# Kernel optimization log

Measured on AMD Instinct MI355X. Metric: run time of the kernel, lower is better.

## Reference

```python
import jax, jax.numpy as jnp
import numpy as np

B = 8192          # batch of agents
K = 4             # max_neighbors
NUM_LANES = 12
LANE_F = 4        # obs_dim // num_lanes = 48 // 12
HEADS = 4
OUT = 32          # gat_output_dim per head
EMB = HEADS * OUT # 128, gat_per_lane_output / intersection emb dim
HID = 64          # graphsage_hidden_dim
GRU_H = 32        # gru_hidden_dim
ALPHA = 0.2       # leaky relu slope

# Lane cooperation: lanes of the same approach (4 approaches x 3 lanes) cooperate.
_blk = np.kron(np.eye(4), np.ones((3, 3))).astype(np.float32)
LANE_COOP = jnp.asarray(_blk)
LANE_CONF = jnp.asarray(1.0 - _blk)


def _gat_stream(x, W, a_src, a_dst, adj):
    # x: [N, 12, 4]; W: [H, 4, O]; a_*: [H, O]; adj: [12, 12]
    Wh = jnp.einsum('nlf,hfo->nhlo', x, W)                      # [N,H,12,O]
    e_s = jnp.einsum('nhlo,ho->nhl', Wh, a_src)
    e_d = jnp.einsum('nhlo,ho->nhl', Wh, a_dst)
    e = jax.nn.leaky_relu(e_s[..., :, None] + e_d[..., None, :], ALPHA)  # [N,H,12,12]
    e = jnp.where(adj[None, None] > 0, e, jnp.float32(-1e9))
    att = jax.nn.softmax(e, axis=-1)
    out = jnp.einsum('nhij,nhjo->niho', att, Wh)                # [N,12,H,O]
    return jax.nn.elu(out.reshape(out.shape[0], NUM_LANES, EMB))


def _gru_final(xs, Wih, Whh, bih, bhh):
    # xs: [K, B, HID] -> final hidden [B, GRU_H], torch GRU gate convention (r,z,n)
    def step(h, x):
        gi = x @ Wih + bih
        gh = h @ Whh + bhh
        i_r, i_z, i_n = jnp.split(gi, 3, axis=-1)
        h_r, h_z, h_n = jnp.split(gh, 3, axis=-1)
        r = jax.nn.sigmoid(i_r + h_r)
        z = jax.nn.sigmoid(i_z + h_z)
        n = jnp.tanh(i_n + r * h_n)
        return (1.0 - z) * n + z * h, None
    h0 = jnp.zeros((xs.shape[1], Whh.shape[0]), xs.dtype)
    hT, _ = jax.lax.scan(step, h0, xs)
    return hT


def setup_inputs() -> dict:
    key = jax.random.key(0)
    ks = jax.random.split(key, 24)
    rn = lambda k, s: (jax.random.normal(k, s, jnp.float32) * 0.1)
    z = lambda n: jnp.zeros((n,), jnp.float32)
    return {
        'self_features': jax.random.normal(ks[0], (B, 48), jnp.float32),
        'neighbor_features': jax.random.normal(ks[1], (B, K, 48), jnp.float32),
        'neighbor_mask': (jax.random.uniform(ks[2], (B, K)) > 0.25).astype(jnp.float32),
        'neighbor_directions': jax.random.randint(ks[3], (B, K), 0, 4).astype(jnp.float32) * 0.25,
        # dual-stream GAT params
        'W_coop': rn(ks[4], (HEADS, LANE_F, OUT)), 'a_src_coop': rn(ks[5], (HEADS, OUT)), 'a_dst_coop': rn(ks[6], (HEADS, OUT)),
        'W_conf': rn(ks[7], (HEADS, LANE_F, OUT)), 'a_src_conf': rn(ks[8], (HEADS, OUT)), 'a_dst_conf': rn(ks[9], (HEADS, OUT)),
        'W_fuse': rn(ks[10], (2 * EMB, EMB)), 'b_fuse': z(EMB),
        # GraphSAGE neighbor projection (+1 for direction feature)
        'W_proj': rn(ks[11], (EMB + 1, HID)), 'b_proj': z(HID),
        # BiGRU (fwd/bwd), torch layout transposed: Wih [HID,3H], Whh [H,3H]
        'Wih_f': rn(ks[12], (HID, 3 * GRU_H)), 'Whh_f': rn(ks[13], (GRU_H, 3 * GRU_H)), 'bih_f': z(3 * GRU_H), 'bhh_f': z(3 * GRU_H),
        'Wih_b': rn(ks[14], (HID, 3 * GRU_H)), 'Whh_b': rn(ks[15], (GRU_H, 3 * GRU_H)), 'bih_b': z(3 * GRU_H), 'bhh_b': z(3 * GRU_H),
        # combine self + BiGRU summary -> network embedding
        'W_out': rn(ks[16], (EMB + 2 * GRU_H, HID)), 'b_out': z(HID),
    }


def reference(self_features, neighbor_features, neighbor_mask, neighbor_directions,
              W_coop, a_src_coop, a_dst_coop, W_conf, a_src_conf, a_dst_conf,
              W_fuse, b_fuse, W_proj, b_proj,
              Wih_f, Whh_f, bih_f, bhh_f, Wih_b, Whh_b, bih_b, bhh_b,
              W_out, b_out):
    Bc, Kc = neighbor_features.shape[:2]
    # run dual-stream GAT on self + all neighbors in one batch of small lane graphs
    allx = jnp.concatenate([self_features[:, None, :], neighbor_features], axis=1)
    allx = allx.reshape(Bc * (Kc + 1), NUM_LANES, LANE_F)
    coop = _gat_stream(allx, W_coop, a_src_coop, a_dst_coop, LANE_COOP)
    conf = _gat_stream(allx, W_conf, a_src_conf, a_dst_conf, LANE_CONF)
    fused = jax.nn.elu(jnp.concatenate([coop, conf], axis=-1) @ W_fuse + b_fuse)  # [N,12,128]
    emb = fused.mean(axis=1).reshape(Bc, Kc + 1, EMB)  # mean pool over lanes
    self_emb = emb[:, 0]          # [B,128]
    nbr_emb = emb[:, 1:]          # [B,K,128]
    # GraphSAGE projection of neighbors (direction-aware), masked
    nbr_in = jnp.concatenate([nbr_emb, neighbor_directions[..., None]], axis=-1)
    x = jax.nn.relu(nbr_in @ W_proj + b_proj) * neighbor_mask[..., None]  # [B,K,HID]
    xs = jnp.swapaxes(x, 0, 1)    # [K,B,HID]
    h_f = _gru_final(xs, Wih_f, Whh_f, bih_f, bhh_f)
    h_b = _gru_final(xs[::-1], Wih_b, Whh_b, bih_b, bhh_b)
    net = jax.nn.relu(jnp.concatenate([self_emb, h_f, h_b], axis=-1) @ W_out + b_out)  # [B,64]
    return jnp.concatenate([self_emb, net], axis=-1)  # [B,192]
```

## Files before the change

### kernel.cpp

```cpp
#include <hip/hip_runtime.h>
#include <hip/hip_bf16.h>
#include <math.h>

typedef short short8 __attribute__((ext_vector_type(8)));
typedef float f32x4  __attribute__((ext_vector_type(4)));
typedef unsigned short u16x4 __attribute__((ext_vector_type(4)));

__device__ __forceinline__ unsigned short f2b(float f) {
  union { float f; unsigned int u; } x; x.f = f;
  return (unsigned short)((x.u + 0x7FFFu + ((x.u >> 16) & 1u)) >> 16);
}
__device__ __forceinline__ float b2f_u(unsigned short u) {
  union { unsigned int u; float f; } x; x.u = ((unsigned int)u) << 16;
  return x.f;
}
__device__ __forceinline__ unsigned int pkbf(float a, float b) {
  union { __hip_bfloat162 h; unsigned int u; } c;
  c.h = __float22bfloat162_rn(make_float2(a, b));
  return c.u;
}
__device__ __forceinline__ float sigm(float x) { return 1.f / (1.f + __expf(-x)); }
__device__ __forceinline__ float eluf(float v) {
  return v > 0.f ? v : (__expf(v) - 1.f);
}

__global__ __launch_bounds__(256) void prepack_kernel(
    const float* __restrict__ Wf,
    const float* __restrict__ Wc, const float* __restrict__ Wn,
    const float* __restrict__ as_c, const float* __restrict__ ad_c,
    const float* __restrict__ as_n, const float* __restrict__ ad_n,
    const float* __restrict__ Wproj,
    const float* __restrict__ Wih_f, const float* __restrict__ Wih_b,
    const float* __restrict__ Wout,
    const float* __restrict__ Whh_f, const float* __restrict__ Whh_b,
    unsigned short* __restrict__ fragB,
    unsigned short* __restrict__ fragWB,
    float* __restrict__ Wa,
    unsigned short* __restrict__ fragP,
    unsigned short* __restrict__ fragIH,
    unsigned short* __restrict__ fragO,
    unsigned short* __restrict__ fragHH)
{
  int e = blockIdx.x * 256 + threadIdx.x;
  unsigned short tmp[8];
  if (e < 4096) {
    int kb = e >> 9, tile = (e >> 6) & 7, lane = e & 63;
    int n = tile * 16 + (lane & 15);
    int kbase = kb * 32 + (lane >> 4) * 8;
#pragma unroll
    for (int j = 0; j < 8; j++) tmp[j] = f2b(Wf[(kbase + j) * 128 + n]);
    *(short8*)(fragB + e * 8) = *(short8*)tmp;
  } else if (e < 5120) {
    int i = e - 4096;
    int s = i >> 9, tile = (i >> 6) & 7, lane = i & 63;
    int c15 = lane & 15, quad = lane >> 4;
    int n = tile * 16 + c15;
    int h = n >> 5, o = n & 31;
    const float* W = s ? Wn : Wc;
#pragma unroll
    for (int j = 0; j < 8; j++) {
      int k = quad * 8 + j;
      tmp[j] = ((k >> 2) == h) ? f2b(W[h * 128 + (k & 3) * 32 + o])
                               : (unsigned short)0;
    }
    *(short8*)(fragWB + i * 8) = *(short8*)tmp;
  } else if (e < 5184) {
    int i = e - 5120;
    int s = i >> 5, d = (i >> 4) & 1, h = (i >> 2) & 3, f = i & 3;
    const float* W = s ? Wn : Wc;
    const float* a = s ? (d ? ad_n : as_n) : (d ? ad_c : as_c);
    float acc = 0.f;
#pragma unroll
    for (int o = 0; o < 32; o++) acc += W[h * 128 + f * 32 + o] * a[h * 32 + o];
    Wa[i] = acc;
  } else if (e < 6208) {
    int i = e - 5184;
    int kb = i >> 8, nt = (i >> 6) & 3, lane = i & 63;
    int c15 = lane & 15, quad = lane >> 4;
#pragma unroll
    for (int j = 0; j < 8; j++)
      tmp[j] = f2b(Wproj[(kb * 32 + quad * 8 + j) * 64 + nt * 16 + c15]);
    *(short8*)(fragP + i * 8) = *(short8*)tmp;
  } else if (e < 7744) {
    int i = e - 6208;
    int d = (i >= 768), r = i - d * 768;
    int kb = r / 384, nt = (r >> 6) % 6, lane = r & 63;
    int c15 = lane & 15, quad = lane >> 4;
    const float* W = d ? Wih_b : Wih_f;
#pragma unroll
    for (int j = 0; j < 8; j++)
      tmp[j] = f2b(W[(kb * 32 + quad * 8 + j) * 96 + nt * 16 + c15]);
    *(short8*)(fragIH + i * 8) = *(short8*)tmp;
  } else if (e < 9280) {
    int r = e - 7744;
    int kb = r >> 8, nt = (r >> 6) & 3, lane = r & 63;
    int c15 = lane & 15, quad = lane >> 4;
#pragma unroll
    for (int j = 0; j < 8; j++)
      tmp[j] = f2b(Wout[(kb * 32 + quad * 8 + j) * 64 + nt * 16 + c15]);
    *(short8*)(fragO + r * 8) = *(short8*)tmp;
  } else if (e < 10048) {
    int i = e - 9280;
    int d = i / 384, r = i - d * 384;
    int nt = r >> 6, lane = r & 63;
    int c15 = lane & 15, quad = lane >> 4;
    const float* W = d ? Whh_b : Whh_f;
#pragma unroll
    for (int j = 0; j < 8; j++)
      tmp[j] = f2b(W[(quad * 8 + j) * 96 + nt * 16 + c15]);
    *(short8*)(fragHH + i * 8) = *(short8*)tmp;
  }
}

__global__ __launch_bounds__(256) void gat_fuse_kernel(
    const float* __restrict__ self_f, const float* __restrict__ nbr_f,
    const float* __restrict__ Wa,
    const unsigned short* __restrict__ fragWB,
    const unsigned short* __restrict__ fragB,
    const float* __restrict__ b_fuse,
    float* __restrict__ emb)
{
  const int tid = threadIdx.x;
  const int w = tid >> 6, lane = tid & 63, c15 = lane & 15, quad = lane >> 4;
  const int n0 = blockIdx.x * 2;

  __shared__ __align__(16) float sxf[2][12][4];
  __shared__ float sWa[64];
  __shared__ float sed[2][2][4][12];
  __shared__ __align__(16) unsigned short sA[2][2][16][24];
  __shared__ __align__(16) unsigned short scatb[2][16][268];
  __shared__ float sbias[128];

  if (tid < 128) sbias[tid] = b_fuse[tid];
  if (tid < 64) sWa[tid] = Wa[tid];
  if (tid < 96) {
    int nd = tid / 48, f = tid - nd * 48;
    int nn = n0 + nd, b = nn / 5, slot = nn - b * 5;
    float v = (slot == 0) ? self_f[b * 48 + f]
                          : nbr_f[(b * 4 + slot - 1) * 48 + f];
    sxf[nd][f >> 2][f & 3] = v;
  }
  __syncthreads();

  const int g_q = w & 1, s_q = w >> 1;
  if (lane < 48) {
    int h = lane / 12, i = lane - h * 12;
    float es = 0.f, ed = 0.f;
#pragma unroll
    for (int f = 0; f < 4; f++) {
      float xv = sxf[g_q][i][f];
      es += xv * sWa[s_q * 32 + h * 4 + f];
      ed += xv * sWa[s_q * 32 + 16 + h * 4 + f];
    }
    sed[g_q][s_q][h][i] = ed;
    int blk = i / 3;
    float xa0 = 0.f, xa1 = 0.f, xa2 = 0.f, xa3 = 0.f;
    if (s_q == 0) {
      float ev[3];
      float m = -1e30f;
#pragma unroll
      for (int jj = 0; jj < 3; jj++) {
        float e = es + sed[g_q][0][h][blk * 3 + jj];
        e = e > 0.f ? e : 0.2f * e;
        ev[jj] = e;
        m = fmaxf(m, e);
      }
      float sum = 0.f;
#pragma unroll
      for (int jj = 0; jj < 3; jj++) { ev[jj] = __expf(ev[jj] - m); sum += ev[jj]; }
      float inv = 1.f / sum;
#pragma unroll
      for (int jj = 0; jj < 3; jj++) {
        float aj = ev[jj] * inv;
        f32x4 xj = *(const f32x4*)&sxf[g_q][blk * 3 + jj][0];
        xa0 += aj * xj[0]; xa1 += aj * xj[1];
        xa2 += aj * xj[2]; xa3 += aj * xj[3];
      }
    } else {
      float ev[9];
      float m = -1e30f;
#pragma unroll
      for (int jj = 0; jj < 9; jj++) {
        int j = jj < blk * 3 ? jj : jj + 3;
        float e = es + sed[g_q][1][h][j];
        e = e > 0.f ? e : 0.2f * e;
        ev[jj] = e;
        m = fmaxf(m, e);
      }
      float sum = 0.f;
#pragma unroll
      for (int jj = 0; jj < 9; jj++) { ev[jj] = __expf(ev[jj] - m); sum += ev[jj]; }
      float inv = 1.f / sum;
#pragma unroll
      for (int jj = 0; jj < 9; jj++) {
        int j = jj < blk * 3 ? jj : jj + 3;
        float aj = ev[jj] * inv;
        f32x4 xj = *(const f32x4*)&sxf[g_q][j][0];
        xa0 += aj * xj[0]; xa1 += aj * xj[1];
        xa2 += aj * xj[2]; xa3 += aj * xj[3];
      }
    }
    uint2 pk = make_uint2(pkbf(xa0, xa1), pkbf(xa2, xa3));
    *(uint2*)&sA[g_q][s_q][i][h * 4] = pk;
  }

  {
    const int wn3 = w & 1, ws3 = w >> 1;
    const short8 z8 = {0,0,0,0,0,0,0,0};
    short8 a = z8;
    if (quad < 2) a = *(const short8*)&sA[wn3][ws3][c15][quad * 8];
#pragma unroll
    for (int tile = 0; tile < 8; tile++) {
      short8 bw = *(const short8*)(fragWB + ((ws3 * 8 + tile) * 64 + lane) * 8);
      f32x4 c = {0.f, 0.f, 0.f, 0.f};
      c = __builtin_amdgcn_mfma_f32_16x16x32_bf16(a, bw, c, 0, 0, 0);
      if (quad < 3) {
        int co = ws3 * 128 + tile * 16 + c15;
        unsigned int p01 = pkbf(eluf(c[0]), eluf(c[1]));
        unsigned int p23 = pkbf(eluf(c[2]), eluf(c[3]));
        scatb[wn3][quad * 4 + 0][co] = (unsigned short)(p01 & 0xffffu);
        scatb[wn3][quad * 4 + 1][co] = (unsigned short)(p01 >> 16);
        scatb[wn3][quad * 4 + 2][co] = (unsigned short)(p23 & 0xffffu);
        scatb[wn3][quad * 4 + 3][co] = (unsigned short)(p23 >> 16);
      }
    }
  }
  __syncthreads();

  {
    f32x4 acc[2][2];
#pragma unroll
    for (int nd = 0; nd < 2; nd++)
#pragma unroll
      for (int tt = 0; tt < 2; tt++) acc[nd][tt] = (f32x4){0.f,0.f,0.f,0.f};
#pragma unroll
    for (int kb = 0; kb < 8; kb++) {
      short8 a0 = *(const short8*)&scatb[0][c15][kb * 32 + (quad << 3)];
      short8 a1 = *(const short8*)&scatb[1][c15][kb * 32 + (quad << 3)];
#pragma unroll
      for (int tt = 0; tt < 2; tt++) {
        short8 bw = *(const short8*)(fragB + ((kb * 8 + 2 * w + tt) * 64 + lane) * 8);
        acc[0][tt] = __builtin_amdgcn_mfma_f32_16x16x32_bf16(a0, bw, acc[0][tt], 0, 0, 0);
        acc[1][tt] = __builtin_amdgcn_mfma_f32_16x16x32_bf16(a1, bw, acc[1][tt], 0, 0, 0);
      }
    }
    float tot[2][2];
#pragma unroll
    for (int nd = 0; nd < 2; nd++) {
#pragma unroll
      for (int tt = 0; tt < 2; tt++) {
        float p = 0.f;
        if (quad < 3) {
          float bcol = sbias[w * 32 + tt * 16 + c15];
#pragma unroll
          for (int r = 0; r < 4; r++) p += eluf(acc[nd][tt][r] + bcol);
        }
        p += __shfl_xor(p, 16);
        p += __shfl_xor(p, 32);
        tot[nd][tt] = p;
      }
    }
    int ndw = quad >> 1, ttw = quad & 1;
    float val = ndw ? (ttw ? tot[1][1] : tot[1][0])
                    : (ttw ? tot[0][1] : tot[0][0]);
    emb[(n0 + ndw) * 128 + w * 32 + ttw * 16 + c15] = val * (1.f / 12.f);
  }
}

__global__ __launch_bounds__(256) void head_kernel(
    const float* __restrict__ emb,
    const float* __restrict__ maskp, const float* __restrict__ dirsp,
    const float* __restrict__ W_proj, const float* __restrict__ b_proj,
    const unsigned short* __restrict__ fragP,
    const unsigned short* __restrict__ fragIH,
    const unsigned short* __restrict__ fragHH,
    const float* __restrict__ bih_f, const float* __restrict__ bhh_f,
    const float* __restrict__ bih_b, const float* __restrict__ bhh_b,
    const unsigned short* __restrict__ fragO,
    const float* __restrict__ b_out,
    float* __restrict__ out)
{
  const int b8 = blockIdx.x * 8;
  const int tid = threadIdx.x;
  const int w = tid >> 6, lane = tid & 63, c15 = lane & 15, quad = lane >> 4;

  __shared__ __align__(16) unsigned short sX[32][72];
  __shared__ __align__(16) unsigned short sgi[2][32][96];
  __shared__ float sH[2][8][32];
  __shared__ __align__(16) unsigned short sHb[2][16][32];
  __shared__ float sgh[2][8][96];
  __shared__ __align__(16) unsigned short sCat[16][200];
  __shared__ float sPB[128];
  __shared__ float sBI[2][96], sBH[2][96], sBO[64];

  if (tid < 64) { sPB[tid] = b_proj[tid]; sPB[64 + tid] = W_proj[128 * 64 + tid]; sBO[tid] = b_out[tid]; }
  if (tid < 96) { sBI[0][tid] = bih_f[tid]; sBI[1][tid] = bih_b[tid];
                  sBH[0][tid] = bhh_f[tid]; sBH[1][tid] = bhh_b[tid]; }
  {
    unsigned int* hb = (unsigned int*)sHb;
    hb[tid] = 0u; hb[tid + 256] = 0u;
    float* hz = (float*)sH;
    for (int i = tid; i < 512; i += 256) hz[i] = 0.f;
  }
  __syncthreads();

  {
    const int mt = w >> 1;
    const int nt0 = (w & 1) * 2;
    const int sloc = mt * 4 + (c15 >> 2);
    const int nbr  = c15 & 3;
    const float* arow = emb + (((b8 + sloc) * 5) + 1 + nbr) * 128;
    short8 a[4];
#pragma unroll
    for (int kb = 0; kb < 4; kb++) {
      const float* p = arow + kb * 32 + quad * 8;
      f32x4 v0 = *(const f32x4*)p;
      f32x4 v1 = *(const f32x4*)(p + 4);
      unsigned short tmp[8];
      tmp[0]=f2b(v0[0]); tmp[1]=f2b(v0[1]); tmp[2]=f2b(v0[2]); tmp[3]=f2b(v0[3]);
      tmp[4]=f2b(v1[0]); tmp[5]=f2b(v1[1]); tmp[6]=f2b(v1[2]); tmp[7]=f2b(v1[3]);
      a[kb] = *(short8*)tmp;
    }
    f32x4 acc0 = {0.f,0.f,0.f,0.f}, acc1 = acc0;
#pragma unroll
    for (int kb = 0; kb < 4; kb++) {
      short8 b0 = *(const short8*)(fragP + ((kb * 4 + nt0    ) * 64 + lane) * 8);
      short8 b1 = *(const short8*)(fragP + ((kb * 4 + nt0 + 1) * 64 + lane) * 8);
      acc0 = __builtin_amdgcn_mfma_f32_16x16x32_bf16(a[kb], b0, acc0, 0, 0, 0);
      acc1 = __builtin_amdgcn_mfma_f32_16x16x32_bf16(a[kb], b1, acc1, 0, 0, 0);
    }
    const int sE = mt * 4 + quad;
    float dirv[4], maskv[4];
#pragma unroll
    for (int r = 0; r < 4; r++) {
      dirv[r]  = dirsp[(b8 + sE) * 4 + r];
      maskv[r] = maskp[(b8 + sE) * 4 + r];
    }
#pragma unroll
    for (int tt = 0; tt < 2; tt++) {
      f32x4 c = tt ? acc1 : acc0;
      int col = (nt0 + tt) * 16 + c15;
#pragma unroll
      for (int r = 0; r < 4; r++) {
        float v = c[r] + dirv[r] * sPB[64 + col] + sPB[col];
        v = fmaxf(v, 0.f) * maskv[r];
        sX[mt * 16 + quad * 4 + r][col] = f2b(v);
      }
    }
  }
  __syncthreads();

  {
    const int mt = w >> 1;
    const int ntb = (w & 1) * 3;
    short8 a[2];
#pragma unroll
    for (int kb = 0; kb < 2; kb++)
      a[kb] = *(const short8*)&sX[mt * 16 + c15][kb * 32 + quad * 8];
#pragma unroll
    for (int d = 0; d < 2; d++) {
#pragma unroll
      for (int t2 = 0; t2 < 3; t2++) {
        int nt = ntb + t2;
        f32x4 acc = {0.f,0.f,0.f,0.f};
#pragma unroll
        for (int kb = 0; kb < 2; kb++) {
          short8 bb = *(const short8*)(fragIH + ((d * 12 + kb * 6 + nt) * 64 + lane) * 8);
          acc = __builtin_amdgcn_mfma_f32_16x16x32_bf16(a[kb], bb, acc, 0, 0, 0);
        }
        int col = nt * 16 + c15;
        float bi = sBI[d][col];
#pragma unroll
        for (int r = 0; r < 4; r++)
          sgi[d][mt * 16 + quad * 4 + r][col] = f2b(acc[r] + bi);
      }
    }
  }
  __syncthreads();

  if (w < 2) {
    const int d = w;
    const int u = lane & 31, sp = lane >> 5;
    for (int step = 0; step < 4; step++) {
      short8 a = *(const short8*)&sHb[d][c15][quad * 8];
#pragma unroll
      for (int nt = 0; nt < 6; nt++) {
        short8 bb = *(const short8*)(fragHH + ((d * 6 + nt) * 64 + lane) * 8);
        f32x4 c = {0.f,0.f,0.f,0.f};
        c = __builtin_amdgcn_mfma_f32_16x16x32_bf16(a, bb, c, 0, 0, 0);
        if (quad < 2) {
          int col = nt * 16 + c15;
#pragma unroll
          for (int r = 0; r < 4; r++) sgh[d][quad * 4 + r][col] = c[r];
        }
      }
      const int k = d ? (3 - step) : step;
#pragma unroll
      for (int si = 0; si < 4; si++) {
        int s = sp + si * 2;
        int row = s * 4 + k;
        float ghr = sgh[d][s][u]      + sBH[d][u];
        float ghz = sgh[d][s][32 + u] + sBH[d][32 + u];
        float ghn = sgh[d][s][64 + u] + sBH[d][64 + u];
        float r = sigm(b2f_u(sgi[d][row][u]) + ghr);
        float z = sigm(b2f_u(sgi[d][row][32 + u]) + ghz);
        float n = tanhf(b2f_u(sgi[d][row][64 + u]) + r * ghn);
        float h = (1.f - z) * n + z * sH[d][s][u];
        sH[d][s][u] = h;
        sHb[d][s][u] = f2b(h);
        if (step == 3) sCat[s][128 + d * 32 + u] = f2b(h);
      }
    }
  } else {
    for (int i = tid - 128; i < 1024; i += 128) {
      int s = i >> 7, cc = i & 127;
      float v = emb[(b8 + s) * 5 * 128 + cc];
      sCat[s][cc] = f2b(v);
      out[(b8 + s) * 192 + cc] = v;
    }
  }
  __syncthreads();

  {
    const int nt = w;
    f32x4 acc = {0.f,0.f,0.f,0.f};
#pragma unroll
    for (int kb = 0; kb < 6; kb++) {
      short8 a = *(const short8*)&sCat[c15][kb * 32 + quad * 8];
      short8 bb = *(const short8*)(fragO + ((kb * 4 + nt) * 64 + lane) * 8);
      acc = __builtin_amdgcn_mfma_f32_16x16x32_bf16(a, bb, acc, 0, 0, 0);
    }
    if (quad < 2) {
      int col = nt * 16 + c15;
#pragma unroll
      for (int r = 0; r < 4; r++) {
        int m = quad * 4 + r;
        out[(b8 + m) * 192 + 128 + col] = fmaxf(acc[r] + sBO[col], 0.f);
      }
    }
  }
}

extern "C" void kernel_launch(void* const* d_in, const int* in_sizes, int n_in,
                              void* d_out, int out_size, void* d_ws, size_t ws_size,
                              hipStream_t stream) {
  const float* self_f  = (const float*)d_in[0];
  const float* nbr_f   = (const float*)d_in[1];
  const float* maskp   = (const float*)d_in[2];
  const float* dirsp   = (const float*)d_in[3];
  const float* W_coop  = (const float*)d_in[4];
  const float* as_coop = (const float*)d_in[5];
  const float* ad_coop = (const float*)d_in[6];
  const float* W_conf  = (const float*)d_in[7];
  const float* as_conf = (const float*)d_in[8];
  const float* ad_conf = (const float*)d_in[9];
  const float* W_fuse  = (const float*)d_in[10];
  const float* b_fuse  = (const float*)d_in[11];
  const float* W_proj  = (const float*)d_in[12];
  const float* b_proj  = (const float*)d_in[13];
  const float* Wih_f   = (const float*)d_in[14];
  const float* Whh_f   = (const float*)d_in[15];
  const float* bih_f   = (const float*)d_in[16];
  const float* bhh_f   = (const float*)d_in[17];
  const float* Wih_b   = (const float*)d_in[18];
  const float* Whh_b   = (const float*)d_in[19];
  const float* bih_b   = (const float*)d_in[20];
  const float* bhh_b   = (const float*)d_in[21];
  const float* W_out   = (const float*)d_in[22];
  const float* b_out   = (const float*)d_in[23];

  const int B = in_sizes[0] / 48;
  char* ws = (char*)d_ws;
  unsigned short* fragB  = (unsigned short*)(ws);
  unsigned short* fragWB = (unsigned short*)(ws + 65536);
  float*          Wa     = (float*)(ws + 81920);
  unsigned short* fragP  = (unsigned short*)(ws + 82176);
  unsigned short* fragIH = (unsigned short*)(ws + 98560);
  unsigned short* fragO  = (unsigned short*)(ws + 123136);
  unsigned short* fragHH = (unsigned short*)(ws + 147712);
  float*          emb    = (float*)(ws + 160000);

  prepack_kernel<<<40, 256, 0, stream>>>(
      W_fuse, W_coop, W_conf, as_coop, ad_coop, as_conf, ad_conf,
      W_proj, Wih_f, Wih_b, W_out, Whh_f, Whh_b,
      fragB, fragWB, Wa, fragP, fragIH, fragO, fragHH);

  gat_fuse_kernel<<<B * 5 / 2, 256, 0, stream>>>(
      self_f, nbr_f, Wa, fragWB, fragB, b_fuse, emb);

  head_kernel<<<B / 8, 256, 0, stream>>>(
      emb, maskp, dirsp, W_proj, b_proj, fragP, fragIH, fragHH,
      bih_f, bhh_f, bih_b, bhh_b,
      fragO, b_out, (float*)d_out);
}
```

Measured before the change: 231.0 us.

## Store embeddings as bf16, swap MFMA operands for packed stores, vectorize loads, fast tanh

The intermediate embedding buffer becomes bf16, and self embeddings go straight to the output from the GAT kernel, so the head kernel no longer reads and converts fp32. MFMA operand order is swapped in several places so each lane holds contiguous output columns, which allows packed uint2/f32x4 LDS and global stores. The softmax drops its max subtraction and divides once at the end. Input loads become vectorized, and sigmoid/tanh use rcp-based fast approximations. These changes risk exp overflow without the max shift and add bf16 rounding on the self embeddings.

Result: no change. 227.1 us (-1.7%).

```diff
diff --git a/kernel.cpp b/kernel.cpp
--- a/kernel.cpp
+++ b/kernel.cpp
@@ -4,7 +4,6 @@
 
 typedef short short8 __attribute__((ext_vector_type(8)));
 typedef float f32x4  __attribute__((ext_vector_type(4)));
-typedef unsigned short u16x4 __attribute__((ext_vector_type(4)));
 
 __device__ __forceinline__ unsigned short f2b(float f) {
   union { float f; unsigned int u; } x; x.f = f;
@@ -19,7 +18,15 @@
   c.h = __float22bfloat162_rn(make_float2(a, b));
   return c.u;
 }
-__device__ __forceinline__ float sigm(float x) { return 1.f / (1.f + __expf(-x)); }
+__device__ __forceinline__ float sigm(float x) {
+  return __builtin_amdgcn_rcpf(1.f + __expf(-x));
+}
+__device__ __forceinline__ float tanhfast(float x) {
+  float ax = fabsf(x);
+  float em = __expf(-2.f * ax);
+  float t  = (1.f - em) * __builtin_amdgcn_rcpf(1.f + em);
+  return copysignf(t, x);
+}
 __device__ __forceinline__ float eluf(float v) {
   return v > 0.f ? v : (__expf(v) - 1.f);
 }
@@ -118,111 +125,91 @@
     const unsigned short* __restrict__ fragWB,
     const unsigned short* __restrict__ fragB,
     const float* __restrict__ b_fuse,
-    float* __restrict__ emb)
+    unsigned short* __restrict__ embb,
+    float* __restrict__ out)
 {
   const int tid = threadIdx.x;
   const int w = tid >> 6, lane = tid & 63, c15 = lane & 15, quad = lane >> 4;
   const int n0 = blockIdx.x * 2;
 
   __shared__ __align__(16) float sxf[2][12][4];
-  __shared__ float sWa[64];
+  __shared__ __align__(16) float sWa[64];
   __shared__ float sed[2][2][4][12];
   __shared__ __align__(16) unsigned short sA[2][2][16][24];
   __shared__ __align__(16) unsigned short scatb[2][16][268];
-  __shared__ float sbias[128];
-
-  if (tid < 128) sbias[tid] = b_fuse[tid];
-  if (tid < 64) sWa[tid] = Wa[tid];
-  if (tid < 96) {
-    int nd = tid / 48, f = tid - nd * 48;
+  __shared__ __align__(16) float sbias[128];
+
+  if (tid < 32) ((f32x4*)sbias)[tid] = ((const f32x4*)b_fuse)[tid];
+  else if (tid < 48) ((f32x4*)sWa)[tid - 32] = ((const f32x4*)Wa)[tid - 32];
+  if (tid < 24) {
+    int nd = (tid >= 12), q = tid - nd * 12;
     int nn = n0 + nd, b = nn / 5, slot = nn - b * 5;
-    float v = (slot == 0) ? self_f[b * 48 + f]
-                          : nbr_f[(b * 4 + slot - 1) * 48 + f];
-    sxf[nd][f >> 2][f & 3] = v;
+    const float* src = slot ? (nbr_f + (b * 4 + slot - 1) * 48)
+                            : (self_f + b * 48);
+    ((f32x4*)&sxf[nd][0][0])[q] = *(const f32x4*)(src + q * 4);
+  }
+  if (tid >= 128) {
+    int t = tid - 128;
+    int g = t >> 6, s = (t >> 5) & 1, i = 12 + ((t >> 3) & 3), cp = t & 7;
+    *(unsigned int*)&sA[g][s][i][cp * 2] = 0u;
   }
   __syncthreads();
 
   const int g_q = w & 1, s_q = w >> 1;
   if (lane < 48) {
     int h = lane / 12, i = lane - h * 12;
-    float es = 0.f, ed = 0.f;
-#pragma unroll
-    for (int f = 0; f < 4; f++) {
-      float xv = sxf[g_q][i][f];
-      es += xv * sWa[s_q * 32 + h * 4 + f];
-      ed += xv * sWa[s_q * 32 + 16 + h * 4 + f];
-    }
+    f32x4 xv  = *(const f32x4*)&sxf[g_q][i][0];
+    f32x4 was = *(const f32x4*)&sWa[s_q * 32 + h * 4];
+    f32x4 wad = *(const f32x4*)&sWa[s_q * 32 + 16 + h * 4];
+    float es = xv[0]*was[0] + xv[1]*was[1] + xv[2]*was[2] + xv[3]*was[3];
+    float ed = xv[0]*wad[0] + xv[1]*wad[1] + xv[2]*wad[2] + xv[3]*wad[3];
     sed[g_q][s_q][h][i] = ed;
-    int blk = i / 3;
-    float xa0 = 0.f, xa1 = 0.f, xa2 = 0.f, xa3 = 0.f;
+    int blk3 = (i / 3) * 3;
+    float xa0 = 0.f, xa1 = 0.f, xa2 = 0.f, xa3 = 0.f, sum = 0.f;
     if (s_q == 0) {
-      float ev[3];
-      float m = -1e30f;
 #pragma unroll
       for (int jj = 0; jj < 3; jj++) {
-        float e = es + sed[g_q][0][h][blk * 3 + jj];
+        int j = blk3 + jj;
+        float e = es + sed[g_q][0][h][j];
         e = e > 0.f ? e : 0.2f * e;
-        ev[jj] = e;
-        m = fmaxf(m, e);
-      }
-      float sum = 0.f;
-#pragma unroll
-      for (int jj = 0; jj < 3; jj++) { ev[jj] = __expf(ev[jj] - m); sum += ev[jj]; }
-      float inv = 1.f / sum;
-#pragma unroll
-      for (int jj = 0; jj < 3; jj++) {
-        float aj = ev[jj] * inv;
-        f32x4 xj = *(const f32x4*)&sxf[g_q][blk * 3 + jj][0];
-        xa0 += aj * xj[0]; xa1 += aj * xj[1];
-        xa2 += aj * xj[2]; xa3 += aj * xj[3];
+        float p = __expf(e);
+        sum += p;
+        f32x4 xj = *(const f32x4*)&sxf[g_q][j][0];
+        xa0 += p * xj[0]; xa1 += p * xj[1];
+        xa2 += p * xj[2]; xa3 += p * xj[3];
       }
     } else {
-      float ev[9];
-      float m = -1e30f;
 #pragma unroll
       for (int jj = 0; jj < 9; jj++) {
-        int j = jj < blk * 3 ? jj : jj + 3;
+        int j = jj < blk3 ? jj : jj + 3;
         float e = es + sed[g_q][1][h][j];
         e = e > 0.f ? e : 0.2f * e;
-        ev[jj] = e;
-        m = fmaxf(m, e);
-      }
-      float sum = 0.f;
-#pragma unroll
-      for (int jj = 0; jj < 9; jj++) { ev[jj] = __expf(ev[jj] - m); sum += ev[jj]; }
-      float inv = 1.f / sum;
-#pragma unroll
-      for (int jj = 0; jj < 9; jj++) {
-        int j = jj < blk * 3 ? jj : jj + 3;
-        float aj = ev[jj] * inv;
+        float p = __expf(e);
+        sum += p;
         f32x4 xj = *(const f32x4*)&sxf[g_q][j][0];
-        xa0 += aj * xj[0]; xa1 += aj * xj[1];
-        xa2 += aj * xj[2]; xa3 += aj * xj[3];
-      }
-    }
-    uint2 pk = make_uint2(pkbf(xa0, xa1), pkbf(xa2, xa3));
+        xa0 += p * xj[0]; xa1 += p * xj[1];
+        xa2 += p * xj[2]; xa3 += p * xj[3];
+      }
+    }
+    float inv = 1.f / sum;
+    uint2 pk = make_uint2(pkbf(xa0 * inv, xa1 * inv),
+                          pkbf(xa2 * inv, xa3 * inv));
     *(uint2*)&sA[g_q][s_q][i][h * 4] = pk;
   }
 
   {
     const int wn3 = w & 1, ws3 = w >> 1;
     const short8 z8 = {0,0,0,0,0,0,0,0};
-    short8 a = z8;
-    if (quad < 2) a = *(const short8*)&sA[wn3][ws3][c15][quad * 8];
+    short8 xb = z8;
+    if (quad < 2) xb = *(const short8*)&sA[wn3][ws3][c15][quad * 8];
 #pragma unroll
     for (int tile = 0; tile < 8; tile++) {
-      short8 bw = *(const short8*)(fragWB + ((ws3 * 8 + tile) * 64 + lane) * 8);
+      short8 aw = *(const short8*)(fragWB + ((ws3 * 8 + tile) * 64 + lane) * 8);
       f32x4 c = {0.f, 0.f, 0.f, 0.f};
-      c = __builtin_amdgcn_mfma_f32_16x16x32_bf16(a, bw, c, 0, 0, 0);
-      if (quad < 3) {
-        int co = ws3 * 128 + tile * 16 + c15;
-        unsigned int p01 = pkbf(eluf(c[0]), eluf(c[1]));
-        unsigned int p23 = pkbf(eluf(c[2]), eluf(c[3]));
-        scatb[wn3][quad * 4 + 0][co] = (unsigned short)(p01 & 0xffffu);
-        scatb[wn3][quad * 4 + 1][co] = (unsigned short)(p01 >> 16);
-        scatb[wn3][quad * 4 + 2][co] = (unsigned short)(p23 & 0xffffu);
-        scatb[wn3][quad * 4 + 3][co] = (unsigned short)(p23 >> 16);
-      }
+      c = __builtin_amdgcn_mfma_f32_16x16x32_bf16(aw, xb, c, 0, 0, 0);
+      uint2 pk = make_uint2(pkbf(eluf(c[0]), eluf(c[1])),
+                            pkbf(eluf(c[2]), eluf(c[3])));
+      *(uint2*)&scatb[wn3][c15][ws3 * 128 + tile * 16 + (quad << 2)] = pk;
     }
   }
   __syncthreads();
@@ -261,14 +248,18 @@
       }
     }
     int ndw = quad >> 1, ttw = quad & 1;
-    float val = ndw ? (ttw ? tot[1][1] : tot[1][0])
-                    : (ttw ? tot[0][1] : tot[0][0]);
-    emb[(n0 + ndw) * 128 + w * 32 + ttw * 16 + c15] = val * (1.f / 12.f);
+    float val = (ndw ? (ttw ? tot[1][1] : tot[1][0])
+                     : (ttw ? tot[0][1] : tot[0][0])) * (1.f / 12.f);
+    int node = n0 + ndw;
+    int col  = w * 32 + ttw * 16 + c15;
+    embb[node * 128 + col] = f2b(val);
+    int bq = node / 5;
+    if (node == bq * 5) out[bq * 192 + col] = val;
   }
 }
 
 __global__ __launch_bounds__(256) void head_kernel(
-    const float* __restrict__ emb,
+    const unsigned short* __restrict__ embb,
     const float* __restrict__ maskp, const float* __restrict__ dirsp,
     const float* __restrict__ W_proj, const float* __restrict__ b_proj,
     const unsigned short* __restrict__ fragP,
@@ -288,10 +279,11 @@
   __shared__ __align__(16) unsigned short sgi[2][32][96];
   __shared__ float sH[2][8][32];
   __shared__ __align__(16) unsigned short sHb[2][16][32];
-  __shared__ float sgh[2][8][96];
+  __shared__ __align__(16) float sgh[2][8][96];
   __shared__ __align__(16) unsigned short sCat[16][200];
-  __shared__ float sPB[128];
-  __shared__ float sBI[2][96], sBH[2][96], sBO[64];
+  __shared__ __align__(16) float sPB[128];
+  __shared__ __align__(16) float sBI[2][96], sBH[2][96];
+  __shared__ __align__(16) float sBO[64];
 
   if (tid < 64) { sPB[tid] = b_proj[tid]; sPB[64 + tid] = W_proj[128 * 64 + tid]; sBO[tid] = b_out[tid]; }
   if (tid < 96) { sBI[0][tid] = bih_f[tid]; sBI[1][tid] = bih_b[tid];
@@ -305,74 +297,60 @@
   __syncthreads();
 
   {
-    const int mt = w >> 1;
+    const int mt  = w >> 1;
     const int nt0 = (w & 1) * 2;
     const int sloc = mt * 4 + (c15 >> 2);
     const int nbr  = c15 & 3;
-    const float* arow = emb + (((b8 + sloc) * 5) + 1 + nbr) * 128;
-    short8 a[4];
+    const unsigned short* brow = embb + (((b8 + sloc) * 5) + 1 + nbr) * 128;
+    short8 xb[4];
+#pragma unroll
+    for (int kb = 0; kb < 4; kb++)
+      xb[kb] = *(const short8*)(brow + kb * 32 + quad * 8);
+    f32x4 acc0 = {0.f,0.f,0.f,0.f}, acc1 = acc0;
 #pragma unroll
     for (int kb = 0; kb < 4; kb++) {
-      const float* p = arow + kb * 32 + quad * 8;
-      f32x4 v0 = *(const f32x4*)p;
-      f32x4 v1 = *(const f32x4*)(p + 4);
-      unsigned short tmp[8];
-      tmp[0]=f2b(v0[0]); tmp[1]=f2b(v0[1]); tmp[2]=f2b(v0[2]); tmp[3]=f2b(v0[3]);
-      tmp[4]=f2b(v1[0]); tmp[5]=f2b(v1[1]); tmp[6]=f2b(v1[2]); tmp[7]=f2b(v1[3]);
-      a[kb] = *(short8*)tmp;
-    }
-    f32x4 acc0 = {0.f,0.f,0.f,0.f}, acc1 = acc0;
-#pragma unroll
-    for (int kb = 0; kb < 4; kb++) {
-      short8 b0 = *(const short8*)(fragP + ((kb * 4 + nt0    ) * 64 + lane) * 8);
-      short8 b1 = *(const short8*)(fragP + ((kb * 4 + nt0 + 1) * 64 + lane) * 8);
-      acc0 = __builtin_amdgcn_mfma_f32_16x16x32_bf16(a[kb], b0, acc0, 0, 0, 0);
-      acc1 = __builtin_amdgcn_mfma_f32_16x16x32_bf16(a[kb], b1, acc1, 0, 0, 0);
-    }
-    const int sE = mt * 4 + quad;
-    float dirv[4], maskv[4];
-#pragma unroll
-    for (int r = 0; r < 4; r++) {
-      dirv[r]  = dirsp[(b8 + sE) * 4 + r];
-      maskv[r] = maskp[(b8 + sE) * 4 + r];
-    }
+      short8 a0 = *(const short8*)(fragP + ((kb * 4 + nt0    ) * 64 + lane) * 8);
+      short8 a1 = *(const short8*)(fragP + ((kb * 4 + nt0 + 1) * 64 + lane) * 8);
+      acc0 = __builtin_amdgcn_mfma_f32_16x16x32_bf16(a0, xb[kb], acc0, 0, 0, 0);
+      acc1 = __builtin_amdgcn_mfma_f32_16x16x32_bf16(a1, xb[kb], acc1, 0, 0, 0);
+    }
+    const float dirv  = dirsp[(b8 + sloc) * 4 + nbr];
+    const float maskv = maskp[(b8 + sloc) * 4 + nbr];
 #pragma unroll
     for (int tt = 0; tt < 2; tt++) {
       f32x4 c = tt ? acc1 : acc0;
-      int col = (nt0 + tt) * 16 + c15;
-#pragma unroll
-      for (int r = 0; r < 4; r++) {
-        float v = c[r] + dirv[r] * sPB[64 + col] + sPB[col];
-        v = fmaxf(v, 0.f) * maskv[r];
-        sX[mt * 16 + quad * 4 + r][col] = f2b(v);
-      }
-    }
-  }
-  __syncthreads();
-
-  {
-    const int mt = w >> 1;
+      int colb = (nt0 + tt) * 16 + (quad << 2);
+      f32x4 wp = *(const f32x4*)&sPB[64 + colb];
+      f32x4 pb = *(const f32x4*)&sPB[colb];
+      float v0 = fmaxf(c[0] + dirv * wp[0] + pb[0], 0.f) * maskv;
+      float v1 = fmaxf(c[1] + dirv * wp[1] + pb[1], 0.f) * maskv;
+      float v2 = fmaxf(c[2] + dirv * wp[2] + pb[2], 0.f) * maskv;
+      float v3 = fmaxf(c[3] + dirv * wp[3] + pb[3], 0.f) * maskv;
+      uint2 pk = make_uint2(pkbf(v0, v1), pkbf(v2, v3));
+      *(uint2*)&sX[mt * 16 + c15][colb] = pk;
+    }
+  }
+  __syncthreads();
+
+  {
+    const int mt  = w >> 1;
     const int ntb = (w & 1) * 3;
-    short8 a[2];
-#pragma unroll
-    for (int kb = 0; kb < 2; kb++)
-      a[kb] = *(const short8*)&sX[mt * 16 + c15][kb * 32 + quad * 8];
+    short8 xb0 = *(const short8*)&sX[mt * 16 + c15][quad * 8];
+    short8 xb1 = *(const short8*)&sX[mt * 16 + c15][32 + quad * 8];
 #pragma unroll
     for (int d = 0; d < 2; d++) {
 #pragma unroll
       for (int t2 = 0; t2 < 3; t2++) {
         int nt = ntb + t2;
         f32x4 acc = {0.f,0.f,0.f,0.f};
-#pragma unroll
-        for (int kb = 0; kb < 2; kb++) {
-          short8 bb = *(const short8*)(fragIH + ((d * 12 + kb * 6 + nt) * 64 + lane) * 8);
-          acc = __builtin_amdgcn_mfma_f32_16x16x32_bf16(a[kb], bb, acc, 0, 0, 0);
-        }
-        int col = nt * 16 + c15;
-        float bi = sBI[d][col];
-#pragma unroll
-        for (int r = 0; r < 4; r++)
-          sgi[d][mt * 16 + quad * 4 + r][col] = f2b(acc[r] + bi);
+        short8 a0 = *(const short8*)(fragIH + ((d * 12 +     nt) * 64 + lane) * 8);
+        short8 a1 = *(const short8*)(fragIH + ((d * 12 + 6 + nt) * 64 + lane) * 8);
+        acc = __builtin_amdgcn_mfma_f32_16x16x32_bf16(a0, xb0, acc, 0, 0, 0);
+        acc = __builtin_amdgcn_mfma_f32_16x16x32_bf16(a1, xb1, acc, 0, 0, 0);
+        f32x4 bi = *(const f32x4*)&sBI[d][nt * 16 + (quad << 2)];
+        uint2 pk = make_uint2(pkbf(acc[0] + bi[0], acc[1] + bi[1]),
+                              pkbf(acc[2] + bi[2], acc[3] + bi[3]));
+        *(uint2*)&sgi[d][mt * 16 + c15][nt * 16 + (quad << 2)] = pk;
       }
     }
   }
@@ -382,17 +360,14 @@
     const int d = w;
     const int u = lane & 31, sp = lane >> 5;
     for (int step = 0; step < 4; step++) {
-      short8 a = *(const short8*)&sHb[d][c15][quad * 8];
+      short8 hb = *(const short8*)&sHb[d][c15][quad * 8];
 #pragma unroll
       for (int nt = 0; nt < 6; nt++) {
-        short8 bb = *(const short8*)(fragHH + ((d * 6 + nt) * 64 + lane) * 8);
+        short8 aw = *(const short8*)(fragHH + ((d * 6 + nt) * 64 + lane) * 8);
         f32x4 c = {0.f,0.f,0.f,0.f};
-        c = __builtin_amdgcn_mfma_f32_16x16x32_bf16(a, bb, c, 0, 0, 0);
-        if (quad < 2) {
-          int col = nt * 16 + c15;
-#pragma unroll
-          for (int r = 0; r < 4; r++) sgh[d][quad * 4 + r][col] = c[r];
-        }
+        c = __builtin_amdgcn_mfma_f32_16x16x32_bf16(aw, hb, c, 0, 0, 0);
+        if (c15 < 8)
+          *(f32x4*)&sgh[d][c15][nt * 16 + (quad << 2)] = c;
       }
       const int k = d ? (3 - step) : step;
 #pragma unroll
@@ -404,7 +379,7 @@
         float ghn = sgh[d][s][64 + u] + sBH[d][64 + u];
         float r = sigm(b2f_u(sgi[d][row][u]) + ghr);
         float z = sigm(b2f_u(sgi[d][row][32 + u]) + ghz);
-        float n = tanhf(b2f_u(sgi[d][row][64 + u]) + r * ghn);
+        float n = tanhfast(b2f_u(sgi[d][row][64 + u]) + r * ghn);
         float h = (1.f - z) * n + z * sH[d][s][u];
         sH[d][s][u] = h;
         sHb[d][s][u] = f2b(h);
@@ -412,12 +387,10 @@
       }
     }
   } else {
-    for (int i = tid - 128; i < 1024; i += 128) {
-      int s = i >> 7, cc = i & 127;
-      float v = emb[(b8 + s) * 5 * 128 + cc];
-      sCat[s][cc] = f2b(v);
-      out[(b8 + s) * 192 + cc] = v;
-    }
+    int t = tid - 128;
+    int s = t >> 4, c8 = (t & 15) * 8;
+    short8 v = *(const short8*)(embb + (b8 + s) * 5 * 128 + c8);
+    *(short8*)&sCat[s][c8] = v;
   }
   __syncthreads();
 
@@ -426,17 +399,18 @@
     f32x4 acc = {0.f,0.f,0.f,0.f};
 #pragma unroll
     for (int kb = 0; kb < 6; kb++) {
-      short8 a = *(const short8*)&sCat[c15][kb * 32 + quad * 8];
-      short8 bb = *(const short8*)(fragO + ((kb * 4 + nt) * 64 + lane) * 8);
-      acc = __builtin_amdgcn_mfma_f32_16x16x32_bf16(a, bb, acc, 0, 0, 0);
-    }
-    if (quad < 2) {
-      int col = nt * 16 + c15;
-#pragma unroll
-      for (int r = 0; r < 4; r++) {
-        int m = quad * 4 + r;
-        out[(b8 + m) * 192 + 128 + col] = fmaxf(acc[r] + sBO[col], 0.f);
-      }
+      short8 bb = *(const short8*)&sCat[c15][kb * 32 + quad * 8];
+      short8 aw = *(const short8*)(fragO + ((kb * 4 + nt) * 64 + lane) * 8);
+      acc = __builtin_amdgcn_mfma_f32_16x16x32_bf16(aw, bb, acc, 0, 0, 0);
+    }
+    if (c15 < 8) {
+      f32x4 bo = *(const f32x4*)&sBO[nt * 16 + (quad << 2)];
+      f32x4 v;
+      v[0] = fmaxf(acc[0] + bo[0], 0.f);
+      v[1] = fmaxf(acc[1] + bo[1], 0.f);
+      v[2] = fmaxf(acc[2] + bo[2], 0.f);
+      v[3] = fmaxf(acc[3] + bo[3], 0.f);
+      *(f32x4*)(out + (b8 + c15) * 192 + 128 + nt * 16 + (quad << 2)) = v;
     }
   }
 }
@@ -478,7 +452,7 @@
   unsigned short* fragIH = (unsigned short*)(ws + 98560);
   unsigned short* fragO  = (unsigned short*)(ws + 123136);
   unsigned short* fragHH = (unsigned short*)(ws + 147712);
-  float*          emb    = (float*)(ws + 160000);
+  unsigned short* embb   = (unsigned short*)(ws + 160000);
 
   prepack_kernel<<<40, 256, 0, stream>>>(
       W_fuse, W_coop, W_conf, as_coop, ad_coop, as_conf, ad_conf,
@@ -486,10 +460,10 @@
       fragB, fragWB, Wa, fragP, fragIH, fragO, fragHH);
 
   gat_fuse_kernel<<<B * 5 / 2, 256, 0, stream>>>(
-      self_f, nbr_f, Wa, fragWB, fragB, b_fuse, emb);
+      self_f, nbr_f, Wa, fragWB, fragB, b_fuse, embb, (float*)d_out);
 
   head_kernel<<<B / 8, 256, 0, stream>>>(
-      emb, maskp, dirsp, W_proj, b_proj, fragP, fragIH, fragHH,
+      embb, maskp, dirsp, W_proj, b_proj, fragP, fragIH, fragHH,
       bih_f, bhh_f, bih_b, bhh_b,
       fragO, b_out, (float*)d_out);
 }
```
